# Performance work log

Measured on AMD Instinct MI355X. Metric: run time of the kernel, lower is better.

The kernel has to match this reference:

```python
import jax, jax.numpy as jnp
import numpy as np

N = 50000
D_IN = 256
OUT = 16
HEADS = 32
GAT_C = OUT  # out_channels + beta_on(=0)


def _gat_conv(x, src, dst, W, att_src, att_dst, bias):
    """PyG GATConv, concat=False (mean over heads), with self-loops already appended."""
    n = x.shape[0]
    xp = (x @ W).reshape(n, HEADS, GAT_C)            # [N,H,C]
    a_s = jnp.einsum('nhc,hc->nh', xp, att_src)       # [N,H]
    a_d = jnp.einsum('nhc,hc->nh', xp, att_dst)       # [N,H]
    e = jax.nn.leaky_relu(a_s[src] + a_d[dst], 0.2)   # [E,H]
    # segment softmax over incoming edges of each dst node
    m = jax.ops.segment_max(e, dst, num_segments=n)
    e = jnp.exp(e - m[dst])
    s = jax.ops.segment_sum(e, dst, num_segments=n)
    alpha = e / (s[dst] + 1e-16)                      # [E,H]
    out = jax.ops.segment_sum(alpha[:, :, None] * xp[src], dst, num_segments=n)  # [N,H,C]
    return out.mean(axis=1) + bias                    # [N,C]


def setup_inputs() -> dict:
    key = jax.random.key(0)
    ks = jax.random.split(key, 16)
    E = 800000
    x = jax.random.normal(ks[0], (N, D_IN), dtype=jnp.float32)
    edge_index = jax.random.randint(ks[1], (2, E), 0, N, dtype=jnp.int64)
    sc = 1.0 / np.sqrt(D_IN)
    W1 = jax.random.normal(ks[2], (D_IN, HEADS * GAT_C), dtype=jnp.float32) * sc
    att_src1 = jax.random.normal(ks[3], (HEADS, GAT_C), dtype=jnp.float32) * 0.1
    att_dst1 = jax.random.normal(ks[4], (HEADS, GAT_C), dtype=jnp.float32) * 0.1
    b1 = jnp.zeros((GAT_C,), dtype=jnp.float32)
    W2 = jax.random.normal(ks[5], (D_IN, HEADS * GAT_C), dtype=jnp.float32) * sc
    att_src2 = jax.random.normal(ks[6], (HEADS, GAT_C), dtype=jnp.float32) * 0.1
    att_dst2 = jax.random.normal(ks[7], (HEADS, GAT_C), dtype=jnp.float32) * 0.1
    b2 = jnp.zeros((GAT_C,), dtype=jnp.float32)
    lin1_w = jax.random.normal(ks[8], (D_IN, 4 * OUT), dtype=jnp.float32) * sc
    lin1_b = jnp.zeros((4 * OUT,), dtype=jnp.float32)
    lin2_w = jax.random.normal(ks[9], (4 * OUT, OUT), dtype=jnp.float32) * (1.0 / np.sqrt(4 * OUT))
    lin2_b = jnp.zeros((OUT,), dtype=jnp.float32)
    return {"x": x, "edge_index": edge_index,
            "W1": W1, "att_src1": att_src1, "att_dst1": att_dst1, "b1": b1,
            "W2": W2, "att_src2": att_src2, "att_dst2": att_dst2, "b2": b2,
            "lin1_w": lin1_w, "lin1_b": lin1_b, "lin2_w": lin2_w, "lin2_b": lin2_b}


def reference(x, edge_index, W1, att_src1, att_dst1, b1, W2, att_src2, att_dst2, b2,
              lin1_w, lin1_b, lin2_w, lin2_b):
    n = x.shape[0]
    loops = jnp.arange(n, dtype=edge_index.dtype)
    # conv1: flow source_to_target on edge_index -> aggregate src=row0 into dst=row1
    src = jnp.concatenate([edge_index[0], loops])
    dst = jnp.concatenate([edge_index[1], loops])
    x_in = jax.nn.elu(_gat_conv(x, src, dst, W1, att_src1, att_dst1, b1))
    # conv2: flow target_to_source on transposed edge_index -> same effective (src,dst)
    x_out = jax.nn.elu(_gat_conv(x, src, dst, W2, att_src2, att_dst2, b2))
    x1 = jax.nn.elu(x @ lin1_w + lin1_b)
    x_self = jax.nn.elu(x1 @ lin2_w + lin2_b)
    return (x_in, x_out, x_self)
```

## Files before the change

### kernel.cpp

```cpp
#include <hip/hip_runtime.h>

typedef __bf16 bf16x8 __attribute__((ext_vector_type(8)));
typedef float  f32x4  __attribute__((ext_vector_type(4)));
typedef float  f32x2  __attribute__((ext_vector_type(2)));

#define NNODES   50000
#define DIN      256
#define HEADS    32
#define CDIM     16
#define NH       512
#define ERAW     800000
#define SCAN_B   196
#define LDSW     280
#define LOG2E    1.4426950408889634f

#if __has_builtin(__builtin_amdgcn_exp2f)
#define EXP2(x) __builtin_amdgcn_exp2f(x)
#else
#define EXP2(x) __expf((x) * 0.6931471805599453f)
#endif

__device__ __forceinline__ float b2f(unsigned short u) {
    return __uint_as_float(((unsigned)u) << 16);
}
__device__ __forceinline__ unsigned short f2b(float f) {
    unsigned v = __float_as_uint(f);
    v += 0x7fffu + ((v >> 16) & 1u);
    return (unsigned short)(v >> 16);
}

__global__ void k_detect(const int* __restrict__ ei, int* __restrict__ flag) {
    if (threadIdx.x == 0 && blockIdx.x == 0) {
        int nz = 0;
        #pragma unroll
        for (int t = 0; t < 64; ++t) nz |= ei[2 * t + 1];
        flag[0] = (nz == 0) ? 1 : 0;
    }
}

__global__ void k_zero_deg(int* __restrict__ deg) {
    int i = blockIdx.x * 256 + threadIdx.x;
    if (i < NNODES) deg[i] = 0;
}

__global__ void k_hist(const int* __restrict__ ei, const int* __restrict__ flag,
                       int* __restrict__ deg) {
    int e = blockIdx.x * 256 + threadIdx.x;
    int d = flag[0] ? ei[2 * ERAW + 2 * e] : ei[ERAW + e];
    atomicAdd(&deg[d], 1);
}

__global__ void k_scan_blk(const int* __restrict__ deg, int* __restrict__ part,
                           int* __restrict__ bsum) {
    __shared__ int sm[256];
    int b = blockIdx.x, t = threadIdx.x, i = b * 256 + t;
    int v = (i < NNODES) ? deg[i] : 0;
    sm[t] = v; __syncthreads();
    for (int off = 1; off < 256; off <<= 1) {
        int u = (t >= off) ? sm[t - off] : 0;
        __syncthreads();
        sm[t] += u; __syncthreads();
    }
    if (i < NNODES) part[i] = sm[t] - v;
    if (t == 255) bsum[b] = sm[255];
}

__global__ void k_scan_top(int* __restrict__ bsum) {
    __shared__ int sm[256];
    int t = threadIdx.x;
    int v = (t < SCAN_B) ? bsum[t] : 0;
    sm[t] = v; __syncthreads();
    for (int off = 1; off < 256; off <<= 1) {
        int u = (t >= off) ? sm[t - off] : 0;
        __syncthreads();
        sm[t] += u; __syncthreads();
    }
    if (t < SCAN_B) bsum[t] = sm[t] - v;
}

__global__ void k_scan_add(const int* __restrict__ part, const int* __restrict__ bsum,
                           int* __restrict__ rs, int* __restrict__ cur) {
    int b = blockIdx.x, t = threadIdx.x, i = b * 256 + t;
    if (i < NNODES) { int r = part[i] + bsum[b]; rs[i] = r; cur[i] = r; }
}

__global__ void k_scatter(const int* __restrict__ ei, const int* __restrict__ flag,
                          int* __restrict__ cur, int* __restrict__ csr) {
    int e = blockIdx.x * 256 + threadIdx.x;
    int s, d;
    if (flag[0]) { s = ei[2 * e]; d = ei[2 * ERAW + 2 * e]; }
    else         { s = ei[e];     d = ei[ERAW + e]; }
    int pos = atomicAdd(&cur[d], 1);
    csr[pos] = s;
}

__global__ void k_cast_x(const float* __restrict__ x, unsigned short* __restrict__ xb) {
    int i = blockIdx.x * 256 + threadIdx.x;
    float4 v = *(const float4*)(x + (size_t)i * 4);
    ushort4 o;
    o.x = f2b(v.x); o.y = f2b(v.y); o.z = f2b(v.z); o.w = f2b(v.w);
    *(ushort4*)(xb + (size_t)i * 4) = o;
}

__global__ void k_tr(const float* __restrict__ src, unsigned short* __restrict__ dst,
                     int K, int N) {
    int n = blockIdx.x, k = threadIdx.x;
    dst[n * K + k] = f2b(src[k * N + n]);
}

__global__ void k_trT(const float* __restrict__ src, unsigned short* __restrict__ dst,
                      int srcStride, int doPi) {
    __shared__ unsigned short T[64][258];
    int n0 = blockIdx.x * 64;
    int t = threadIdx.x;
    int nl = (t & 15) * 4;
    int kr = t >> 4;
    for (int kk = 0; kk < 256; kk += 16) {
        int k = kk + kr;
        float4 v = *(const float4*)(src + (size_t)k * srcStride + n0 + nl);
        T[nl + 0][k] = f2b(v.x);
        T[nl + 1][k] = f2b(v.y);
        T[nl + 2][k] = f2b(v.z);
        T[nl + 3][k] = f2b(v.w);
    }
    __syncthreads();
    int rl = t >> 2;
    int pr = doPi ? (((rl & 15) << 2) | (rl >> 4)) : rl;
    #pragma unroll
    for (int j = 0; j < 16; ++j) {
        int c4 = (t & 3) + 4 * j;
        ushort2 o0 = *(const ushort2*)&T[pr][c4 * 4];
        ushort2 o1 = *(const ushort2*)&T[pr][c4 * 4 + 2];
        ushort4 o; o.x = o0.x; o.y = o0.y; o.z = o1.x; o.w = o1.y;
        *(ushort4*)(dst + ((size_t)(n0 + rl)) * DIN + c4 * 4) = o;
    }
}

__global__ void __launch_bounds__(256)
k_gemm_xp(const unsigned short* __restrict__ xb,
          const unsigned short* __restrict__ Wt,
          unsigned* __restrict__ xp8,
          const float* __restrict__ att_src, const float* __restrict__ att_dst,
          float* __restrict__ a_s, float* __restrict__ a_d) {
    __shared__ unsigned short As[64 * LDSW];
    int row0 = blockIdx.x * 64;
    int tid = threadIdx.x;
    int w = tid >> 6, lane = tid & 63;
    int r = lane & 15, quad = lane >> 4;

    {
        int row = tid >> 2, slot = tid & 3;
        const uint4* g = (const uint4*)(xb + (size_t)(row0 + row) * DIN);
        uint4* l = (uint4*)(As + row * LDSW);
        #pragma unroll
        for (int i = 0; i < 8; ++i)
            l[slot + 4 * i] = g[slot + 4 * i];
    }
    __syncthreads();

    const f32x4* As4 = (const f32x4*)att_src;
    const f32x4* Ad4 = (const f32x4*)att_dst;

    #pragma unroll
    for (int ch = 0; ch < 2; ++ch) {
        f32x4 acc[4][4] = {};
        #pragma unroll
        for (int kc = 0; kc < 8; ++kc) {
            bf16x8 a[4], b[4];
            #pragma unroll
            for (int sub = 0; sub < 4; ++sub)
                a[sub] = *(const bf16x8*)(As + (sub * 16 + r) * LDSW + kc * 32 + quad * 8);
            #pragma unroll
            for (int t = 0; t < 4; ++t) {
                int col = ch * 256 + w * 64 + t * 16 + r;
                b[t] = *(const bf16x8*)(Wt + (size_t)col * DIN + kc * 32 + quad * 8);
            }
            #pragma unroll
            for (int t = 0; t < 4; ++t)
                #pragma unroll
                for (int sub = 0; sub < 4; ++sub)
                    acc[sub][t] = __builtin_amdgcn_mfma_f32_16x16x32_bf16(a[sub], b[t], acc[sub][t], 0, 0, 0);
        }
        int h = ch * 16 + w * 4 + (r >> 2);
        f32x4 sc = As4[h * 4 + (r & 3)];
        f32x4 dc = Ad4[h * 4 + (r & 3)];
        #pragma unroll
        for (int sub = 0; sub < 4; ++sub) {
            #pragma unroll
            for (int j = 0; j < 4; ++j) {
                int row = row0 + sub * 16 + quad * 4 + j;
                if (row < NNODES) {
                    unsigned u = (unsigned)__builtin_amdgcn_cvt_pk_fp8_f32(
                                     acc[sub][0][j], acc[sub][1][j], 0, false);
                    u = (unsigned)__builtin_amdgcn_cvt_pk_fp8_f32(
                                     acc[sub][2][j], acc[sub][3][j], (int)u, true);
                    xp8[(size_t)row * 128 + ch * 64 + w * 16 + r] = u;
                }
            }
            f32x4 ps = acc[sub][0] * sc.x + acc[sub][1] * sc.y
                     + acc[sub][2] * sc.z + acc[sub][3] * sc.w;
            f32x4 pd = acc[sub][0] * dc.x + acc[sub][1] * dc.y
                     + acc[sub][2] * dc.z + acc[sub][3] * dc.w;
            #pragma unroll
            for (int m = 1; m <= 2; m <<= 1) {
                #pragma unroll
                for (int c = 0; c < 4; ++c) {
                    ps[c] += __shfl_xor(ps[c], m, 64);
                    pd[c] += __shfl_xor(pd[c], m, 64);
                }
            }
            int j = r & 3;
            int row = row0 + sub * 16 + quad * 4 + j;
            if (row < NNODES) {
                a_s[row * HEADS + h] = ps[j] * LOG2E;
                a_d[row * HEADS + h] = pd[j] * LOG2E;
            }
        }
    }
}

__global__ void k_conv(const int* __restrict__ csr, const int* __restrict__ rs,
                       const int* __restrict__ deg,
                       const unsigned* __restrict__ xp8,
                       const float* __restrict__ a_s, const float* __restrict__ a_d,
                       const float* __restrict__ bias, float* __restrict__ out) {
    int nd = blockIdx.x * 4 + (threadIdx.x >> 6);
    int ln = threadIdx.x & 63;
    int h  = ln >> 1;
    int cb = (ln & 1) * 8;
    float adn = a_d[nd * HEADS + h];
    int beg = __builtin_amdgcn_readfirstlane(rs[nd]);
    int cnt = __builtin_amdgcn_readfirstlane(deg[nd]);
    const uint2* xv = (const uint2*)xp8;

    float denom = 0.f;
    float acc[8] = {0, 0, 0, 0, 0, 0, 0, 0};

    #define EDGE_BODY(AV, QV, LIVE)                                        \
    {                                                                      \
        float tt = (AV) + adn;                                             \
        tt = fmaxf(tt, 0.2f * tt);                                         \
        float e = EXP2(tt);                                                \
        e = (LIVE) ? e : 0.f;                                              \
        denom += e;                                                        \
        f32x2 p0 = __builtin_amdgcn_cvt_pk_f32_fp8((int)(QV).x, false);    \
        f32x2 p1 = __builtin_amdgcn_cvt_pk_f32_fp8((int)(QV).x, true);     \
        f32x2 p2 = __builtin_amdgcn_cvt_pk_f32_fp8((int)(QV).y, false);    \
        f32x2 p3 = __builtin_amdgcn_cvt_pk_f32_fp8((int)(QV).y, true);     \
        acc[0] += e * p0.x; acc[1] += e * p0.y;                            \
        acc[2] += e * p1.x; acc[3] += e * p1.y;                            \
        acc[4] += e * p2.x; acc[5] += e * p2.y;                            \
        acc[6] += e * p3.x; acc[7] += e * p3.y;                            \
    }

    float avS = a_s[nd * HEADS + h];
    uint2 qvS = xv[(size_t)nd * 64 + ln];
    int nb = (cnt + 3) >> 2;
    float avP[4]; uint2 qvP[4]; int svN[4];
    if (nb > 0) {
        #pragma unroll
        for (int k = 0; k < 4; ++k) {
            int ce = k < cnt ? k : cnt - 1;
            int s = csr[beg + ce];
            avP[k] = a_s[s * HEADS + h];
            qvP[k] = xv[(size_t)s * 64 + ln];
        }
        #pragma unroll
        for (int k = 0; k < 4; ++k) {
            int idx = 4 + k;
            int ce = idx < cnt ? idx : cnt - 1;
            svN[k] = csr[beg + ce];
        }
    }
    __builtin_amdgcn_sched_barrier(0);
    EDGE_BODY(avS, qvS, 1)

    for (int b = 1; b < nb; ++b) {
        float avN[4]; uint2 qvN[4];
        #pragma unroll
        for (int k = 0; k < 4; ++k) {
            int s = svN[k];
            avN[k] = a_s[s * HEADS + h];
            qvN[k] = xv[(size_t)s * 64 + ln];
        }
        {
            int nbase = (b + 1 < nb ? b + 1 : nb - 1) * 4;
            #pragma unroll
            for (int k = 0; k < 4; ++k) {
                int idx = nbase + k;
                int ce = idx < cnt ? idx : cnt - 1;
                svN[k] = csr[beg + ce];
            }
        }
        __builtin_amdgcn_sched_barrier(0);
        #pragma unroll
        for (int k = 0; k < 4; ++k) EDGE_BODY(avP[k], qvP[k], 1)
        #pragma unroll
        for (int k = 0; k < 4; ++k) { avP[k] = avN[k]; qvP[k] = qvN[k]; }
    }
    if (nb > 0) {
        #pragma unroll
        for (int k = 0; k < 4; ++k) {
            int idx = (nb - 1) * 4 + k;
            EDGE_BODY(avP[k], qvP[k], idx < cnt)
        }
    }
    #undef EDGE_BODY

    float inv = 1.f / (denom + 1e-16f);
    #pragma unroll
    for (int c = 0; c < 8; ++c) acc[c] *= inv;

    #pragma unroll
    for (int mask = 2; mask <= 32; mask <<= 1) {
        #pragma unroll
        for (int c = 0; c < 8; ++c) acc[c] += __shfl_xor(acc[c], mask, 64);
    }
    if (ln < 2) {
        #pragma unroll
        for (int c2 = 0; c2 < 8; ++c2) {
            int c = cb + c2;
            float o = acc[c2] * (1.0f / HEADS) + bias[c];
            out[(size_t)nd * CDIM + c] = o > 0.f ? o : expm1f(o);
        }
    }
}

__global__ void k_mlp1(const unsigned short* __restrict__ xb,
                       const unsigned short* __restrict__ w1t,
                       const float* __restrict__ bb1, unsigned short* __restrict__ x1) {
    int wave = blockIdx.x * 4 + (threadIdx.x >> 6);
    if (wave >= 782) return;
    int lane = threadIdx.x & 63;
    int r = lane & 15, quad = lane >> 4;
    int row0 = wave * 64;

    f32x4 acc[4][4] = {};
    #pragma unroll
    for (int kc = 0; kc < 8; ++kc) {
        bf16x8 a[4];
        #pragma unroll
        for (int sub = 0; sub < 4; ++sub) {
            int row = row0 + sub * 16 + r;
            if (row0 + sub * 16 < NNODES)
                a[sub] = *(const bf16x8*)(xb + (size_t)row * DIN + kc * 32 + quad * 8);
            else {
                union { unsigned short u[8]; bf16x8 v; } z;
                #pragma unroll
                for (int j = 0; j < 8; ++j) z.u[j] = 0;
                a[sub] = z.v;
            }
        }
        #pragma unroll
        for (int t = 0; t < 4; ++t) {
            int col = t * 16 + r;
            bf16x8 b = *(const bf16x8*)(w1t + (size_t)col * DIN + kc * 32 + quad * 8);
            #pragma unroll
            for (int sub = 0; sub < 4; ++sub)
                acc[sub][t] = __builtin_amdgcn_mfma_f32_16x16x32_bf16(a[sub], b, acc[sub][t], 0, 0, 0);
        }
    }
    #pragma unroll
    for (int sub = 0; sub < 4; ++sub) {
        #pragma unroll
        for (int t = 0; t < 4; ++t) {
            int col = t * 16 + r;
            float bv = bb1[col];
            #pragma unroll
            for (int j = 0; j < 4; ++j) {
                int row = row0 + sub * 16 + quad * 4 + j;
                if (row < NNODES) {
                    float v = acc[sub][t][j] + bv;
                    v = v > 0.f ? v : expm1f(v);
                    x1[(size_t)row * 64 + col] = f2b(v);
                }
            }
        }
    }
}

__global__ void k_mlp2(const unsigned short* __restrict__ x1,
                       const unsigned short* __restrict__ w2t,
                       const float* __restrict__ bb2, float* __restrict__ out) {
    int wave = blockIdx.x * 4 + (threadIdx.x >> 6);
    if (wave >= 3125) return;
    int lane = threadIdx.x & 63;
    int r = lane & 15, quad = lane >> 4;

    f32x4 acc = {};
    #pragma unroll
    for (int kc = 0; kc < 2; ++kc) {
        bf16x8 a = *(const bf16x8*)(x1 + (size_t)(wave * 16 + r) * 64 + kc * 32 + quad * 8);
        bf16x8 b = *(const bf16x8*)(w2t + (size_t)r * 64 + kc * 32 + quad * 8);
        acc = __builtin_amdgcn_mfma_f32_16x16x32_bf16(a, b, acc, 0, 0, 0);
    }
    float bv = bb2[r];
    #pragma unroll
    for (int j = 0; j < 4; ++j) {
        int row = wave * 16 + quad * 4 + j;
        float v = acc[j] + bv;
        v = v > 0.f ? v : expm1f(v);
        out[(size_t)row * CDIM + r] = v;
    }
}

extern "C" void kernel_launch(void* const* d_in, const int* in_sizes, int n_in,
                              void* d_out, int out_size, void* d_ws, size_t ws_size,
                              hipStream_t stream) {
    const float* x  = (const float*)d_in[0];
    const int* ei   = (const int*)d_in[1];
    const float* W[2]    = {(const float*)d_in[2], (const float*)d_in[6]};
    const float* atS[2]  = {(const float*)d_in[3], (const float*)d_in[7]};
    const float* atD[2]  = {(const float*)d_in[4], (const float*)d_in[8]};
    const float* bias[2] = {(const float*)d_in[5], (const float*)d_in[9]};
    const float* w1 = (const float*)d_in[10];
    const float* b1 = (const float*)d_in[11];
    const float* w2 = (const float*)d_in[12];
    const float* b2 = (const float*)d_in[13];
    float* out = (float*)d_out;

    char* ws = (char*)d_ws;
    unsigned* xp8 = (unsigned*)(ws);
    unsigned short* xb  = (unsigned short*)(ws + 25600000);
    unsigned short* Wt  = (unsigned short*)(ws + 51200000);
    unsigned short* w1t = (unsigned short*)(ws + 51462144);
    unsigned short* w2t = (unsigned short*)(ws + 51494912);
    float* a_s = (float*)(ws + 51496960);
    float* a_d = (float*)(ws + 57896960);
    unsigned short* x1 = (unsigned short*)(ws + 51496960);
    int* deg   = (int*)(ws + 64296960);
    int* rs    = (int*)(ws + 64496960);
    int* cur   = (int*)(ws + 64696960);
    int* part  = (int*)(ws + 64896960);
    int* bsum  = (int*)(ws + 65096960);
    int* csr   = (int*)(ws + 65097984);
    int* flag  = (int*)(ws + 68297984);

    k_detect<<<1, 64, 0, stream>>>(ei, flag);
    k_zero_deg<<<SCAN_B, 256, 0, stream>>>(deg);
    k_hist    <<<3125, 256, 0, stream>>>(ei, flag, deg);
    k_scan_blk<<<SCAN_B, 256, 0, stream>>>(deg, part, bsum);
    k_scan_top<<<1, 256, 0, stream>>>(bsum);
    k_scan_add<<<SCAN_B, 256, 0, stream>>>(part, bsum, rs, cur);
    k_scatter <<<3125, 256, 0, stream>>>(ei, flag, cur, csr);

    k_cast_x<<<12500, 256, 0, stream>>>(x, xb);
    k_trT<<<1, 256, 0, stream>>>(w1, w1t, 64, 0);
    k_tr<<<16, 64, 0, stream>>>(w2, w2t, 64, CDIM);

    for (int cv = 0; cv < 2; ++cv) {
        k_trT    <<<8, 256, 0, stream>>>(W[cv], Wt, NH, 1);
        k_gemm_xp<<<782, 256, 0, stream>>>(xb, Wt, xp8, atS[cv], atD[cv], a_s, a_d);
        k_conv   <<<12500, 256, 0, stream>>>(csr, rs, deg, xp8, a_s, a_d,
                                             bias[cv], out + (size_t)cv * 800000);
    }
    k_mlp1<<<196, 256, 0, stream>>>(xb, w1t, b1, x1);
    k_mlp2<<<782, 256, 0, stream>>>(x1, w2t, b2, out + 1600000);
}
```

Baseline: 490.6 us.

## Fuse prep kernels, drop scan_add, and fuse the two MLP layers

Merges detect, zero-degree, x cast and all weight transposes (both GAT weights at once) into one k_prep launch. Removes k_scan_add by having scatter and conv compute row starts as part[d]+bsum[d>>8], with cur zeroed in k_prep. Fuses mlp1 and mlp2 so the hidden activations stay in LDS instead of a global round trip. This cuts launch count and some global traffic, at the cost of an extra lookup per edge in scatter and more LDS use in the MLP kernel.

```diff
diff --git a/kernel.cpp b/kernel.cpp
--- a/kernel.cpp
+++ b/kernel.cpp
@@ -13,6 +13,8 @@
 #define SCAN_B   196
 #define LDSW     280
 #define LOG2E    1.4426950408889634f
+#define CAST_B   12500
+#define PREP_B   (CAST_B + SCAN_B + 18)
 
 #if __has_builtin(__builtin_amdgcn_exp2f)
 #define EXP2(x) __builtin_amdgcn_exp2f(x)
@@ -29,18 +31,70 @@
     return (unsigned short)(v >> 16);
 }
 
-__global__ void k_detect(const int* __restrict__ ei, int* __restrict__ flag) {
-    if (threadIdx.x == 0 && blockIdx.x == 0) {
-        int nz = 0;
-        #pragma unroll
-        for (int t = 0; t < 64; ++t) nz |= ei[2 * t + 1];
-        flag[0] = (nz == 0) ? 1 : 0;
-    }
-}
-
-__global__ void k_zero_deg(int* __restrict__ deg) {
-    int i = blockIdx.x * 256 + threadIdx.x;
-    if (i < NNODES) deg[i] = 0;
+__global__ void __launch_bounds__(256) k_prep(
+        const float* __restrict__ x, unsigned short* __restrict__ xb,
+        const float* __restrict__ W0, const float* __restrict__ W1,
+        const float* __restrict__ w1, const float* __restrict__ w2,
+        unsigned short* __restrict__ Wt2, unsigned short* __restrict__ w1t,
+        unsigned short* __restrict__ w2t,
+        const int* __restrict__ ei, int* __restrict__ flag,
+        int* __restrict__ deg, int* __restrict__ cur) {
+    __shared__ unsigned short T[64][258];
+    int bid = blockIdx.x, t = threadIdx.x;
+
+    if (bid < CAST_B) {
+        int i = bid * 256 + t;
+        float4 v = *(const float4*)(x + (size_t)i * 4);
+        ushort4 o;
+        o.x = f2b(v.x); o.y = f2b(v.y); o.z = f2b(v.z); o.w = f2b(v.w);
+        *(ushort4*)(xb + (size_t)i * 4) = o;
+        return;
+    }
+    if (bid < CAST_B + SCAN_B) {
+        int i = (bid - CAST_B) * 256 + t;
+        if (i < NNODES) { deg[i] = 0; cur[i] = 0; }
+        if (bid == CAST_B && t == 0) {
+            int nz = 0;
+            #pragma unroll
+            for (int k = 0; k < 64; ++k) nz |= ei[2 * k + 1];
+            flag[0] = (nz == 0) ? 1 : 0;
+        }
+        return;
+    }
+    int tb = bid - (CAST_B + SCAN_B);
+    if (tb == 17) {
+        for (int idx = t; idx < 1024; idx += 256) {
+            int n = idx >> 6, k = idx & 63;
+            w2t[n * 64 + k] = f2b(w2[k * CDIM + n]);
+        }
+        return;
+    }
+    const float* src; unsigned short* dst; int srcStride, doPi, tile;
+    if (tb < 8)       { src = W0; dst = Wt2;             srcStride = NH; doPi = 1; tile = tb; }
+    else if (tb < 16) { src = W1; dst = Wt2 + 512 * DIN; srcStride = NH; doPi = 1; tile = tb - 8; }
+    else              { src = w1; dst = w1t;             srcStride = 64; doPi = 0; tile = 0; }
+    int n0 = tile * 64;
+    int nl = (t & 15) * 4;
+    int kr = t >> 4;
+    for (int kk = 0; kk < 256; kk += 16) {
+        int k = kk + kr;
+        float4 v = *(const float4*)(src + (size_t)k * srcStride + n0 + nl);
+        T[nl + 0][k] = f2b(v.x);
+        T[nl + 1][k] = f2b(v.y);
+        T[nl + 2][k] = f2b(v.z);
+        T[nl + 3][k] = f2b(v.w);
+    }
+    __syncthreads();
+    int rl = t >> 2;
+    int pr = doPi ? (((rl & 15) << 2) | (rl >> 4)) : rl;
+    #pragma unroll
+    for (int j = 0; j < 16; ++j) {
+        int c4 = (t & 3) + 4 * j;
+        ushort2 o0 = *(const ushort2*)&T[pr][c4 * 4];
+        ushort2 o1 = *(const ushort2*)&T[pr][c4 * 4 + 2];
+        ushort4 o; o.x = o0.x; o.y = o0.y; o.z = o1.x; o.w = o1.y;
+        *(ushort4*)(dst + ((size_t)(n0 + rl)) * DIN + c4 * 4) = o;
+    }
 }
 
 __global__ void k_hist(const int* __restrict__ ei, const int* __restrict__ flag,
@@ -78,62 +132,15 @@
     if (t < SCAN_B) bsum[t] = sm[t] - v;
 }
 
-__global__ void k_scan_add(const int* __restrict__ part, const int* __restrict__ bsum,
-                           int* __restrict__ rs, int* __restrict__ cur) {
-    int b = blockIdx.x, t = threadIdx.x, i = b * 256 + t;
-    if (i < NNODES) { int r = part[i] + bsum[b]; rs[i] = r; cur[i] = r; }
-}
-
 __global__ void k_scatter(const int* __restrict__ ei, const int* __restrict__ flag,
+                          const int* __restrict__ part, const int* __restrict__ bsum,
                           int* __restrict__ cur, int* __restrict__ csr) {
     int e = blockIdx.x * 256 + threadIdx.x;
     int s, d;
     if (flag[0]) { s = ei[2 * e]; d = ei[2 * ERAW + 2 * e]; }
     else         { s = ei[e];     d = ei[ERAW + e]; }
-    int pos = atomicAdd(&cur[d], 1);
+    int pos = part[d] + bsum[d >> 8] + atomicAdd(&cur[d], 1);
     csr[pos] = s;
-}
-
-__global__ void k_cast_x(const float* __restrict__ x, unsigned short* __restrict__ xb) {
-    int i = blockIdx.x * 256 + threadIdx.x;
-    float4 v = *(const float4*)(x + (size_t)i * 4);
-    ushort4 o;
-    o.x = f2b(v.x); o.y = f2b(v.y); o.z = f2b(v.z); o.w = f2b(v.w);
-    *(ushort4*)(xb + (size_t)i * 4) = o;
-}
-
-__global__ void k_tr(const float* __restrict__ src, unsigned short* __restrict__ dst,
-                     int K, int N) {
-    int n = blockIdx.x, k = threadIdx.x;
-    dst[n * K + k] = f2b(src[k * N + n]);
-}
-
-__global__ void k_trT(const float* __restrict__ src, unsigned short* __restrict__ dst,
-                      int srcStride, int doPi) {
-    __shared__ unsigned short T[64][258];
-    int n0 = blockIdx.x * 64;
-    int t = threadIdx.x;
-    int nl = (t & 15) * 4;
-    int kr = t >> 4;
-    for (int kk = 0; kk < 256; kk += 16) {
-        int k = kk + kr;
-        float4 v = *(const float4*)(src + (size_t)k * srcStride + n0 + nl);
-        T[nl + 0][k] = f2b(v.x);
-        T[nl + 1][k] = f2b(v.y);
-        T[nl + 2][k] = f2b(v.z);
-        T[nl + 3][k] = f2b(v.w);
-    }
-    __syncthreads();
-    int rl = t >> 2;
-    int pr = doPi ? (((rl & 15) << 2) | (rl >> 4)) : rl;
-    #pragma unroll
-    for (int j = 0; j < 16; ++j) {
-        int c4 = (t & 3) + 4 * j;
-        ushort2 o0 = *(const ushort2*)&T[pr][c4 * 4];
-        ushort2 o1 = *(const ushort2*)&T[pr][c4 * 4 + 2];
-        ushort4 o; o.x = o0.x; o.y = o0.y; o.z = o1.x; o.w = o1.y;
-        *(ushort4*)(dst + ((size_t)(n0 + rl)) * DIN + c4 * 4) = o;
-    }
 }
 
 __global__ void __launch_bounds__(256)
@@ -219,8 +226,8 @@
     }
 }
 
-__global__ void k_conv(const int* __restrict__ csr, const int* __restrict__ rs,
-                       const int* __restrict__ deg,
+__global__ void k_conv(const int* __restrict__ csr, const int* __restrict__ part,
+                       const int* __restrict__ bsum, const int* __restrict__ deg,
                        const unsigned* __restrict__ xp8,
                        const float* __restrict__ a_s, const float* __restrict__ a_d,
                        const float* __restrict__ bias, float* __restrict__ out) {
@@ -229,7 +236,8 @@
     int h  = ln >> 1;
     int cb = (ln & 1) * 8;
     float adn = a_d[nd * HEADS + h];
-    int beg = __builtin_amdgcn_readfirstlane(rs[nd]);
+    int beg = __builtin_amdgcn_readfirstlane(part[nd])
+            + __builtin_amdgcn_readfirstlane(bsum[nd >> 8]);
     int cnt = __builtin_amdgcn_readfirstlane(deg[nd]);
     const uint2* xv = (const uint2*)xp8;
 
@@ -326,10 +334,13 @@
     }
 }
 
-__global__ void k_mlp1(const unsigned short* __restrict__ xb,
-                       const unsigned short* __restrict__ w1t,
-                       const float* __restrict__ bb1, unsigned short* __restrict__ x1) {
-    int wave = blockIdx.x * 4 + (threadIdx.x >> 6);
+__global__ void __launch_bounds__(256)
+k_mlp(const unsigned short* __restrict__ xb, const unsigned short* __restrict__ w1t,
+      const float* __restrict__ bb1, const unsigned short* __restrict__ w2t,
+      const float* __restrict__ bb2, float* __restrict__ out) {
+    __shared__ unsigned short T[4][64][72];
+    int wv = threadIdx.x >> 6;
+    int wave = blockIdx.x * 4 + wv;
     if (wave >= 782) return;
     int lane = threadIdx.x & 63;
     int r = lane & 15, quad = lane >> 4;
@@ -368,39 +379,33 @@
             float bv = bb1[col];
             #pragma unroll
             for (int j = 0; j < 4; ++j) {
-                int row = row0 + sub * 16 + quad * 4 + j;
-                if (row < NNODES) {
-                    float v = acc[sub][t][j] + bv;
-                    v = v > 0.f ? v : expm1f(v);
-                    x1[(size_t)row * 64 + col] = f2b(v);
-                }
-            }
-        }
-    }
-}
-
-__global__ void k_mlp2(const unsigned short* __restrict__ x1,
-                       const unsigned short* __restrict__ w2t,
-                       const float* __restrict__ bb2, float* __restrict__ out) {
-    int wave = blockIdx.x * 4 + (threadIdx.x >> 6);
-    if (wave >= 3125) return;
-    int lane = threadIdx.x & 63;
-    int r = lane & 15, quad = lane >> 4;
-
-    f32x4 acc = {};
-    #pragma unroll
-    for (int kc = 0; kc < 2; ++kc) {
-        bf16x8 a = *(const bf16x8*)(x1 + (size_t)(wave * 16 + r) * 64 + kc * 32 + quad * 8);
-        bf16x8 b = *(const bf16x8*)(w2t + (size_t)r * 64 + kc * 32 + quad * 8);
-        acc = __builtin_amdgcn_mfma_f32_16x16x32_bf16(a, b, acc, 0, 0, 0);
-    }
-    float bv = bb2[r];
-    #pragma unroll
-    for (int j = 0; j < 4; ++j) {
-        int row = wave * 16 + quad * 4 + j;
-        float v = acc[j] + bv;
-        v = v > 0.f ? v : expm1f(v);
-        out[(size_t)row * CDIM + r] = v;
+                float v = acc[sub][t][j] + bv;
+                v = v > 0.f ? v : expm1f(v);
+                T[wv][sub * 16 + quad * 4 + j][col] = f2b(v);
+            }
+        }
+    }
+    f32x4 acc2[4] = {};
+    #pragma unroll
+    for (int sub = 0; sub < 4; ++sub) {
+        #pragma unroll
+        for (int kc = 0; kc < 2; ++kc) {
+            bf16x8 a = *(const bf16x8*)&T[wv][sub * 16 + r][kc * 32 + quad * 8];
+            bf16x8 b = *(const bf16x8*)(w2t + r * 64 + kc * 32 + quad * 8);
+            acc2[sub] = __builtin_amdgcn_mfma_f32_16x16x32_bf16(a, b, acc2[sub], 0, 0, 0);
+        }
+    }
+    float bv2 = bb2[r];
+    #pragma unroll
+    for (int sub = 0; sub < 4; ++sub) {
+        #pragma unroll
+        for (int j = 0; j < 4; ++j) {
+            int row = row0 + sub * 16 + quad * 4 + j;
+            if (row < NNODES) {
+                float v = acc2[sub][j] + bv2;
+                out[(size_t)row * CDIM + r] = v > 0.f ? v : expm1f(v);
+            }
+        }
     }
 }
 
@@ -422,38 +427,30 @@
     char* ws = (char*)d_ws;
     unsigned* xp8 = (unsigned*)(ws);
     unsigned short* xb  = (unsigned short*)(ws + 25600000);
-    unsigned short* Wt  = (unsigned short*)(ws + 51200000);
-    unsigned short* w1t = (unsigned short*)(ws + 51462144);
-    unsigned short* w2t = (unsigned short*)(ws + 51494912);
-    float* a_s = (float*)(ws + 51496960);
-    float* a_d = (float*)(ws + 57896960);
-    unsigned short* x1 = (unsigned short*)(ws + 51496960);
-    int* deg   = (int*)(ws + 64296960);
-    int* rs    = (int*)(ws + 64496960);
-    int* cur   = (int*)(ws + 64696960);
-    int* part  = (int*)(ws + 64896960);
-    int* bsum  = (int*)(ws + 65096960);
-    int* csr   = (int*)(ws + 65097984);
-    int* flag  = (int*)(ws + 68297984);
-
-    k_detect<<<1, 64, 0, stream>>>(ei, flag);
-    k_zero_deg<<<SCAN_B, 256, 0, stream>>>(deg);
+    unsigned short* Wt2 = (unsigned short*)(ws + 51200000);
+    unsigned short* w1t = (unsigned short*)(ws + 51724288);
+    unsigned short* w2t = (unsigned short*)(ws + 51757056);
+    float* a_s = (float*)(ws + 51759104);
+    float* a_d = (float*)(ws + 58159104);
+    int* deg   = (int*)(ws + 64559104);
+    int* cur   = (int*)(ws + 64759104);
+    int* part  = (int*)(ws + 64959104);
+    int* bsum  = (int*)(ws + 65159104);
+    int* csr   = (int*)(ws + 65160128);
+    int* flag  = (int*)(ws + 68360128);
+
+    k_prep    <<<PREP_B, 256, 0, stream>>>(x, xb, W[0], W[1], w1, w2,
+                                           Wt2, w1t, w2t, ei, flag, deg, cur);
     k_hist    <<<3125, 256, 0, stream>>>(ei, flag, deg);
     k_scan_blk<<<SCAN_B, 256, 0, stream>>>(deg, part, bsum);
     k_scan_top<<<1, 256, 0, stream>>>(bsum);
-    k_scan_add<<<SCAN_B, 256, 0, stream>>>(part, bsum, rs, cur);
-    k_scatter <<<3125, 256, 0, stream>>>(ei, flag, cur, csr);
-
-    k_cast_x<<<12500, 256, 0, stream>>>(x, xb);
-    k_trT<<<1, 256, 0, stream>>>(w1, w1t, 64, 0);
-    k_tr<<<16, 64, 0, stream>>>(w2, w2t, 64, CDIM);
+    k_scatter <<<3125, 256, 0, stream>>>(ei, flag, part, bsum, cur, csr);
 
     for (int cv = 0; cv < 2; ++cv) {
-        k_trT    <<<8, 256, 0, stream>>>(W[cv], Wt, NH, 1);
-        k_gemm_xp<<<782, 256, 0, stream>>>(xb, Wt, xp8, atS[cv], atD[cv], a_s, a_d);
-        k_conv   <<<12500, 256, 0, stream>>>(csr, rs, deg, xp8, a_s, a_d,
+        k_gemm_xp<<<782, 256, 0, stream>>>(xb, Wt2 + (size_t)cv * 512 * DIN,
+                                           xp8, atS[cv], atD[cv], a_s, a_d);
+        k_conv   <<<12500, 256, 0, stream>>>(csr, part, bsum, deg, xp8, a_s, a_d,
                                              bias[cv], out + (size_t)cv * 800000);
     }
-    k_mlp1<<<196, 256, 0, stream>>>(xb, w1t, b1, x1);
-    k_mlp2<<<782, 256, 0, stream>>>(x1, w2t, b2, out + 1600000);
-}
+    k_mlp<<<196, 256, 0, stream>>>(xb, w1t, b1, w2t, b2, out + 1600000);
+}
```

Result: faster. 461.2 us (-6.0%).
